# Performance work log

Measured on AMD Instinct MI355X. Metric: run time of the kernel, lower is better.

The kernel has to match this reference:

```python
import jax, jax.numpy as jnp
import numpy as np

IMAGE_SIZE = (128, 128)
NUM_SLICES = 4
SLICE_SPACING = 0.1
BACKGROUND = 0.0
CHUNK = 1024
N_GAUSS = 4096
EPS = 1e-6


def setup_inputs() -> dict:
    key = jax.random.key(0)
    k1, k2, k3, k4, k5 = jax.random.split(key, 5)
    return {
        "means": jax.random.uniform(k1, (N_GAUSS, 3), dtype=jnp.float32),
        "scales": jax.random.uniform(k2, (N_GAUSS, 3), dtype=jnp.float32),
        "rotations": jax.random.normal(k3, (N_GAUSS, 4), dtype=jnp.float32),
        "opacities": jax.random.uniform(k4, (N_GAUSS, 1), dtype=jnp.float32),
        "features": jax.random.uniform(k5, (N_GAUSS, 1), dtype=jnp.float32),
    }


def _quat_to_rot(q):
    # q: [N,4] (w,x,y,z) -> [N,3,3]
    q = q / jnp.linalg.norm(q, axis=1, keepdims=True)
    w, x, y, z = q[:, 0], q[:, 1], q[:, 2], q[:, 3]
    r0 = jnp.stack([1 - 2 * (y * y + z * z), 2 * (x * y - w * z), 2 * (x * z + w * y)], axis=-1)
    r1 = jnp.stack([2 * (x * y + w * z), 1 - 2 * (x * x + z * z), 2 * (y * z - w * x)], axis=-1)
    r2 = jnp.stack([2 * (x * z - w * y), 2 * (y * z + w * x), 1 - 2 * (x * x + y * y)], axis=-1)
    return jnp.stack([r0, r1, r2], axis=-2)


def _forward(means, scales, rotations, opacities, features):
    H, W = IMAGE_SIZE
    dtype = means.dtype
    P = H * W

    # 3D covariance: Sigma = (R S)(R S)^T
    R = _quat_to_rot(rotations)
    RS = R * scales[:, None, :]
    cov = RS @ jnp.swapaxes(RS, 1, 2)  # [N,3,3]

    # slice z positions and shared pixel grid
    total_depth = (NUM_SLICES - 1) * SLICE_SPACING
    zs = jnp.linspace(-total_depth / 2, total_depth / 2, NUM_SLICES)
    yy, xx = jnp.meshgrid(jnp.linspace(-1, 1, H), jnp.linspace(-1, 1, W), indexing="ij")
    grid = jnp.stack([xx, yy], axis=-1).reshape(P, 2).astype(dtype)

    # conditional (marginal-at-z) 2D covariance, slice independent
    sxy = cov[:, :2, :2]                     # [N,2,2]
    sxz = cov[:, :2, 2]                      # [N,2]
    szz = cov[:, 2, 2]                       # [N]
    sigma2d = sxy - (sxz[:, :, None] * sxz[:, None, :]) / (szz + EPS)[:, None, None]
    sigma2d = sigma2d + EPS * jnp.eye(2, dtype=dtype)
    a, b = sigma2d[:, 0, 0], sigma2d[:, 0, 1]
    c, d = sigma2d[:, 1, 0], sigma2d[:, 1, 1]
    det = a * d - b * c
    inv2d = jnp.stack([jnp.stack([d, -b], -1), jnp.stack([-c, a], -1)], -2) / det[:, None, None]

    max_dist = 3.0 * scales[:, 2].max()

    nch = N_GAUSS // CHUNK
    rs = lambda t: t.reshape((nch, CHUNK) + t.shape[1:])
    chunks = (rs(means), rs(inv2d), rs(sxz), rs(szz), rs(opacities[:, 0]), rs(features[:, 0]))

    def render_slice(slice_z):
        def body(carry, ch):
            img, acc = carry
            mu, invk, sxzk, szzk, op, ft = ch
            mask = (jnp.abs(mu[:, 2] - slice_z) < max_dist).astype(dtype)  # all-pass by construction
            zoff = slice_z - mu[:, 2]
            mu2d = mu[:, :2] + sxzk / (szzk + EPS)[:, None] * zoff[:, None]  # [K,2]
            off = grid[:, None, :] - mu2d[None, :, :]                        # [P,K,2]
            maha = jnp.einsum("pki,kij,pkj->pk", off, invk, off)
            g = jnp.exp(-0.5 * maha) * mask[None, :]                         # [P,K]
            weight = (1 - acc)[:, None] * (g * op[None, :])
            img = img + (weight * (g * ft[None, :])).sum(-1)
            acc = acc + weight.sum(-1)
            return (img, acc), None

        init = (jnp.zeros(P, dtype), jnp.zeros(P, dtype))
        (img, acc), _ = jax.lax.scan(body, init, chunks)
        img = img + (1 - acc) * BACKGROUND
        return img.reshape(H, W)

    return jnp.stack([render_slice(zs[s]) for s in range(NUM_SLICES)], axis=0)


def reference(means, scales, rotations, opacities, features):
    return _forward(means, scales, rotations, opacities, features)
```

## Files before the change

### kernel.cpp

```cpp
#include <hip/hip_runtime.h>


#define EPSV 1e-6f
#define NG   4096
#define PP   16384
#define NSL  4
#define SPLIT 8
#define PXW  64
#define GPW  128

__global__ void prep_kernel(const float* __restrict__ means,
                            const float* __restrict__ scales,
                            const float* __restrict__ rots,
                            const float* __restrict__ ops,
                            const float* __restrict__ fts,
                            float4* __restrict__ gdata) {
    __shared__ float red[256];
    int tid = threadIdx.x;

    float m = -1e30f;
    for (int i = tid; i < NG; i += 256) m = fmaxf(m, scales[i*3+2]);
    red[tid] = m;
    __syncthreads();
    for (int s = 128; s > 0; s >>= 1) {
        if (tid < s) red[tid] = fmaxf(red[tid], red[tid+s]);
        __syncthreads();
    }
    float maxd = 3.0f * red[0];

    int g = blockIdx.x * 256 + tid;
    if (g >= NG) return;

    float qw = rots[g*4+0], qx = rots[g*4+1], qy = rots[g*4+2], qz = rots[g*4+3];
    float inorm = rsqrtf(qw*qw + qx*qx + qy*qy + qz*qz);
    qw *= inorm; qx *= inorm; qy *= inorm; qz *= inorm;

    float s0 = scales[g*3+0], s1 = scales[g*3+1], s2 = scales[g*3+2];

    float r00 = 1.f - 2.f*(qy*qy + qz*qz), r01 = 2.f*(qx*qy - qw*qz), r02 = 2.f*(qx*qz + qw*qy);
    float r10 = 2.f*(qx*qy + qw*qz), r11 = 1.f - 2.f*(qx*qx + qz*qz), r12 = 2.f*(qy*qz - qw*qx);
    float r20 = 2.f*(qx*qz - qw*qy), r21 = 2.f*(qy*qz + qw*qx), r22 = 1.f - 2.f*(qx*qx + qy*qy);

    float a00 = r00*s0, a01 = r01*s1, a02 = r02*s2;
    float a10 = r10*s0, a11 = r11*s1, a12 = r12*s2;
    float a20 = r20*s0, a21 = r21*s1, a22 = r22*s2;

    float c00 = a00*a00 + a01*a01 + a02*a02;
    float c01 = a00*a10 + a01*a11 + a02*a12;
    float c02 = a00*a20 + a01*a21 + a02*a22;
    float c11 = a10*a10 + a11*a11 + a12*a12;
    float c12 = a10*a20 + a11*a21 + a12*a22;
    float c22 = a20*a20 + a21*a21 + a22*a22;

    float izz = 1.0f / (c22 + EPSV);
    float kx = c02 * izz, ky = c12 * izz;
    float sa = c00 - c02*c02*izz + EPSV;
    float sb = c01 - c02*c12*izz;
    float sd = c11 - c12*c12*izz + EPSV;
    float det = sa*sd - sb*sb;
    float idet = 1.0f / det;

    const float C0 = -0.72134752044448170f;
    float qa = C0 * sd * idet;
    float qb = C0 * (-2.0f * sb * idet);
    float qd = C0 * sa * idet;

    float mx = means[g*3+0], my = means[g*3+1], mz = means[g*3+2];
    float op = ops[g], ft = fts[g];

    #pragma unroll
    for (int s = 0; s < NSL; ++s) {
        float z = -0.15f + 0.1f * (float)s;
        float zoff = z - mz;
        float m2x = mx + kx * zoff;
        float m2y = my + ky * zoff;
        bool live = (fabsf(mz - z) < maxd) && (op > 1e-12f);
        float lop  = live ? __log2f(op) : -__builtin_inff();
        float ftop = live ? ft / op     : 0.f;
        gdata[(s*NG + g)*2 + 0] = make_float4(m2x, m2y, qa, qb);
        gdata[(s*NG + g)*2 + 1] = make_float4(qd, lop, ftop, 0.f);
    }
}

__global__ __launch_bounds__(512, 8)
void render_kernel(const float4* __restrict__ gdata, float* __restrict__ out) {
    __shared__ float parts[SPLIT][PXW][9];

    int tid   = threadIdx.x;
    int px    = tid & 63;
    int split = __builtin_amdgcn_readfirstlane(tid >> 6);
    int slice = blockIdx.x >> 8;
    int tile  = blockIdx.x & 255;
    int pxg   = tile * PXW + px;
    int row   = pxg >> 7, col = pxg & 127;
    float x = (float)col * (2.0f/127.0f) - 1.0f;
    float y = (float)row * (2.0f/127.0f) - 1.0f;

    const float4* gs = gdata + slice * (NG*2);

    #pragma unroll
    for (int c = 0; c < 4; ++c) {
        const float4* p = gs + (size_t)(c*1024 + split*GPW) * 2;
        float a1 = 0.f, a2 = 0.f;
        #pragma unroll 8
        for (int g = 0; g < GPW; ++g) {
            float4 A = p[2*g+0];
            float4 B = p[2*g+1];
            float dx = x - A.x;
            float dy = y - A.y;
            float t  = fmaf(A.z, dx, A.w * dy);
            float e  = fmaf(B.x * dy, dy, B.y);
            float mm = fmaf(dx, t, e);
            float gv = __builtin_amdgcn_exp2f(mm);
            a1 += gv;
            a2 = fmaf(gv * gv, B.z, a2);
        }
        parts[split][px][c]     = a1;
        parts[split][px][c + 4] = a2;
    }
    __syncthreads();

    if (tid < 64) {
        float img = 0.f, acc = 0.f;
        #pragma unroll
        for (int c = 0; c < 4; ++c) {
            float S1 = 0.f, S2 = 0.f;
            #pragma unroll
            for (int s = 0; s < SPLIT; ++s) {
                S1 += parts[s][px][c];
                S2 += parts[s][px][c + 4];
            }
            float om = 1.0f - acc;
            img = fmaf(om, S2, img);
            acc = fmaf(om, S1, acc);
        }
        out[slice * PP + pxg] = img;
    }
}

extern "C" void kernel_launch(void* const* d_in, const int* in_sizes, int n_in,
                              void* d_out, int out_size, void* d_ws, size_t ws_size,
                              hipStream_t stream) {
    const float* means  = (const float*)d_in[0];
    const float* scales = (const float*)d_in[1];
    const float* rots   = (const float*)d_in[2];
    const float* ops    = (const float*)d_in[3];
    const float* fts    = (const float*)d_in[4];
    float* out = (float*)d_out;

    float4* gdata = (float4*)d_ws;

    prep_kernel<<<NG/256, 256, 0, stream>>>(means, scales, rots, ops, fts, gdata);
    render_kernel<<<NSL*(PP/PXW), 512, 0, stream>>>(gdata, out);
}
```

Measured before the change: 147.7 us.

## Render two pixels per thread with packed float2 math and duplicated Gaussian params

Each thread now handles two pixels in the same row, 64 columns apart, and does the per-Gaussian math on 2-wide float vectors. The aim is to let the compiler emit packed FP32 instructions (v_pk_fma/v_pk_add), halving the ALU instruction count per pixel. The prep kernel stores every parameter duplicated into float2 pairs and negates the means so vector loads feed the packed ops directly. This doubles the Gaussian data footprint (64 bytes per Gaussian per slice) and halves the block count to 512. The launch-bounds occupancy hint is also dropped.

```diff
diff --git a/kernel.cpp b/kernel.cpp
--- a/kernel.cpp
+++ b/kernel.cpp
@@ -6,8 +6,9 @@
 #define PP   16384
 #define NSL  4
 #define SPLIT 8
-#define PXW  64
 #define GPW  128
+
+typedef float v2f __attribute__((ext_vector_type(2)));
 
 __global__ void prep_kernel(const float* __restrict__ means,
                             const float* __restrict__ scales,
@@ -77,64 +78,78 @@
         bool live = (fabsf(mz - z) < maxd) && (op > 1e-12f);
         float lop  = live ? __log2f(op) : -__builtin_inff();
         float ftop = live ? ft / op     : 0.f;
-        gdata[(s*NG + g)*2 + 0] = make_float4(m2x, m2y, qa, qb);
-        gdata[(s*NG + g)*2 + 1] = make_float4(qd, lop, ftop, 0.f);
+        float4* o = gdata + ((size_t)(s*NG + g)) * 4;
+        o[0] = make_float4(-m2x, -m2x, -m2y, -m2y);
+        o[1] = make_float4( qa,   qa,   qb,   qb );
+        o[2] = make_float4( qd,   qd,   lop,  lop);
+        o[3] = make_float4( ftop, ftop, 0.f,  0.f);
     }
 }
 
-__global__ __launch_bounds__(512, 8)
-void render_kernel(const float4* __restrict__ gdata, float* __restrict__ out) {
-    __shared__ float parts[SPLIT][PXW][9];
+__global__ __launch_bounds__(512)
+void render_kernel(const v2f* __restrict__ gdata, float* __restrict__ out) {
+    __shared__ float parts[SPLIT][64][20];
 
     int tid   = threadIdx.x;
-    int px    = tid & 63;
+    int lane  = tid & 63;
     int split = __builtin_amdgcn_readfirstlane(tid >> 6);
-    int slice = blockIdx.x >> 8;
-    int tile  = blockIdx.x & 255;
-    int pxg   = tile * PXW + px;
-    int row   = pxg >> 7, col = pxg & 127;
-    float x = (float)col * (2.0f/127.0f) - 1.0f;
-    float y = (float)row * (2.0f/127.0f) - 1.0f;
+    int slice = blockIdx.x >> 7;
+    int row   = blockIdx.x & 127;
 
-    const float4* gs = gdata + slice * (NG*2);
+    const float DL = 2.0f / 127.0f;
+    float xlo = -1.0f + (float)lane * DL;
+    float y   = -1.0f + (float)row  * DL;
+    v2f xP; xP.x = xlo; xP.y = xlo + 64.0f * DL;
+    v2f yP; yP.x = y;   yP.y = y;
+
+    const v2f* gs = gdata + (size_t)slice * NG * 8;
 
     #pragma unroll
     for (int c = 0; c < 4; ++c) {
-        const float4* p = gs + (size_t)(c*1024 + split*GPW) * 2;
-        float a1 = 0.f, a2 = 0.f;
-        #pragma unroll 8
+        const v2f* p = gs + (size_t)(c * 1024 + split * GPW) * 8;
+        v2f a1 = {0.f, 0.f}, a2 = {0.f, 0.f};
+        #pragma unroll 4
         for (int g = 0; g < GPW; ++g) {
-            float4 A = p[2*g+0];
-            float4 B = p[2*g+1];
-            float dx = x - A.x;
-            float dy = y - A.y;
-            float t  = fmaf(A.z, dx, A.w * dy);
-            float e  = fmaf(B.x * dy, dy, B.y);
-            float mm = fmaf(dx, t, e);
-            float gv = __builtin_amdgcn_exp2f(mm);
+            const v2f* q = p + g * 8;
+            v2f nmx = q[0], nmy = q[1], qa = q[2], qb = q[3];
+            v2f qd  = q[4], lop = q[5], ftp = q[6];
+            v2f dx = xP + nmx;
+            v2f dy = yP + nmy;
+            v2f e  = __builtin_elementwise_fma(qd * dy, dy, lop);
+            v2f t  = __builtin_elementwise_fma(qa, dx, qb * dy);
+            v2f mm = __builtin_elementwise_fma(dx, t, e);
+            v2f gv;
+            gv.x = __builtin_amdgcn_exp2f(mm.x);
+            gv.y = __builtin_amdgcn_exp2f(mm.y);
             a1 += gv;
-            a2 = fmaf(gv * gv, B.z, a2);
+            a2 = __builtin_elementwise_fma(gv * gv, ftp, a2);
         }
-        parts[split][px][c]     = a1;
-        parts[split][px][c + 4] = a2;
+        parts[split][lane][c*4+0] = a1.x;
+        parts[split][lane][c*4+1] = a1.y;
+        parts[split][lane][c*4+2] = a2.x;
+        parts[split][lane][c*4+3] = a2.y;
     }
     __syncthreads();
 
     if (tid < 64) {
-        float img = 0.f, acc = 0.f;
+        float imgl = 0.f, accl = 0.f, imgh = 0.f, acch = 0.f;
         #pragma unroll
         for (int c = 0; c < 4; ++c) {
-            float S1 = 0.f, S2 = 0.f;
+            float S1l = 0.f, S1h = 0.f, S2l = 0.f, S2h = 0.f;
             #pragma unroll
             for (int s = 0; s < SPLIT; ++s) {
-                S1 += parts[s][px][c];
-                S2 += parts[s][px][c + 4];
+                S1l += parts[s][tid][c*4+0];
+                S1h += parts[s][tid][c*4+1];
+                S2l += parts[s][tid][c*4+2];
+                S2h += parts[s][tid][c*4+3];
             }
-            float om = 1.0f - acc;
-            img = fmaf(om, S2, img);
-            acc = fmaf(om, S1, acc);
+            float oml = 1.f - accl, omh = 1.f - acch;
+            imgl = fmaf(oml, S2l, imgl);  accl = fmaf(oml, S1l, accl);
+            imgh = fmaf(omh, S2h, imgh);  acch = fmaf(omh, S1h, acch);
         }
-        out[slice * PP + pxg] = img;
+        int base = slice * PP + row * 128;
+        out[base + tid]      = imgl;
+        out[base + tid + 64] = imgh;
     }
 }
 
@@ -151,5 +166,5 @@
     float4* gdata = (float4*)d_ws;
 
     prep_kernel<<<NG/256, 256, 0, stream>>>(means, scales, rots, ops, fts, gdata);
-    render_kernel<<<NSL*(PP/PXW), 512, 0, stream>>>(gdata, out);
+    render_kernel<<<NSL*128, 512, 0, stream>>>((const v2f*)gdata, out);
 }
```

Result: slower. 157.0 us (+6.3%).

## Register-block four pixels per thread with packed float2 math and 16-way split

Applied to the files above, without the earlier changes.

Each thread now evaluates four pixels (two columns by two rows) per loaded Gaussian using packed two-wide float vector ops. This amortises the shared Gaussian loads and the x/y offset math across pixels. Blocks grow to 1024 threads covering two image rows, with the Gaussian range split 16 ways, and the per-chunk reduction is spread over four waves instead of one. Means are stored negated so the offset becomes an add. The costs are more registers per thread, an extra barrier per chunk, and only 256 blocks in the grid, which may leave the device under-occupied.

```diff
diff --git a/kernel.cpp b/kernel.cpp
--- a/kernel.cpp
+++ b/kernel.cpp
@@ -5,9 +5,12 @@
 #define NG   4096
 #define PP   16384
 #define NSL  4
-#define SPLIT 8
-#define PXW  64
-#define GPW  128
+#define SPLIT 16
+#define GPC  64
+
+typedef float v2f __attribute__((ext_vector_type(2)));
+
+static __device__ __forceinline__ v2f splat(float s) { v2f r; r.x = s; r.y = s; return r; }
 
 __global__ void prep_kernel(const float* __restrict__ means,
                             const float* __restrict__ scales,
@@ -77,65 +80,83 @@
         bool live = (fabsf(mz - z) < maxd) && (op > 1e-12f);
         float lop  = live ? __log2f(op) : -__builtin_inff();
         float ftop = live ? ft / op     : 0.f;
-        gdata[(s*NG + g)*2 + 0] = make_float4(m2x, m2y, qa, qb);
-        gdata[(s*NG + g)*2 + 1] = make_float4(qd, lop, ftop, 0.f);
+        float4* o = gdata + ((size_t)(s*NG + g)) * 2;
+        o[0] = make_float4(-m2x, -m2y, qa, qb);
+        o[1] = make_float4( qd,   lop,  ftop, 0.f);
     }
 }
 
-__global__ __launch_bounds__(512, 8)
+__global__ __launch_bounds__(1024, 4)
 void render_kernel(const float4* __restrict__ gdata, float* __restrict__ out) {
-    __shared__ float parts[SPLIT][PXW][9];
+    __shared__ float parts[SPLIT][64][9];
 
     int tid   = threadIdx.x;
-    int px    = tid & 63;
+    int lane  = tid & 63;
     int split = __builtin_amdgcn_readfirstlane(tid >> 6);
-    int slice = blockIdx.x >> 8;
-    int tile  = blockIdx.x & 255;
-    int pxg   = tile * PXW + px;
-    int row   = pxg >> 7, col = pxg & 127;
-    float x = (float)col * (2.0f/127.0f) - 1.0f;
-    float y = (float)row * (2.0f/127.0f) - 1.0f;
+    int slice = blockIdx.x >> 6;
+    int r0    = (blockIdx.x & 63) * 2;
 
-    const float4* gs = gdata + slice * (NG*2);
+    const float DL = 2.0f / 127.0f;
+    v2f xP;  xP.x = -1.0f + (float)lane * DL;  xP.y = xP.x + 64.0f * DL;
+    v2f yP0 = splat(-1.0f + (float)r0 * DL);
+    v2f yP1 = splat(-1.0f + (float)(r0 + 1) * DL);
+
+    const float4* gs = gdata + (size_t)slice * NG * 2;
+
+    float img = 0.f, acc = 0.f;
 
     #pragma unroll
     for (int c = 0; c < 4; ++c) {
-        const float4* p = gs + (size_t)(c*1024 + split*GPW) * 2;
-        float a1 = 0.f, a2 = 0.f;
+        const float4* p = gs + (size_t)(c * 1024 + split * GPC) * 2;
+        v2f a10 = {0.f,0.f}, a11 = {0.f,0.f}, a20 = {0.f,0.f}, a21 = {0.f,0.f};
         #pragma unroll 8
-        for (int g = 0; g < GPW; ++g) {
+        for (int g = 0; g < GPC; ++g) {
             float4 A = p[2*g+0];
             float4 B = p[2*g+1];
-            float dx = x - A.x;
-            float dy = y - A.y;
-            float t  = fmaf(A.z, dx, A.w * dy);
-            float e  = fmaf(B.x * dy, dy, B.y);
-            float mm = fmaf(dx, t, e);
-            float gv = __builtin_amdgcn_exp2f(mm);
-            a1 += gv;
-            a2 = fmaf(gv * gv, B.z, a2);
+            v2f dx  = xP  + splat(A.x);
+            v2f dy0 = yP0 + splat(A.y);
+            v2f dy1 = yP1 + splat(A.y);
+            v2f t0  = __builtin_elementwise_fma(splat(A.z), dx, splat(A.w) * dy0);
+            v2f t1  = __builtin_elementwise_fma(splat(A.z), dx, splat(A.w) * dy1);
+            v2f e0  = __builtin_elementwise_fma(splat(B.x) * dy0, dy0, splat(B.y));
+            v2f e1  = __builtin_elementwise_fma(splat(B.x) * dy1, dy1, splat(B.y));
+            v2f mm0 = __builtin_elementwise_fma(dx, t0, e0);
+            v2f mm1 = __builtin_elementwise_fma(dx, t1, e1);
+            v2f gv0, gv1;
+            gv0.x = __builtin_amdgcn_exp2f(mm0.x);
+            gv0.y = __builtin_amdgcn_exp2f(mm0.y);
+            gv1.x = __builtin_amdgcn_exp2f(mm1.x);
+            gv1.y = __builtin_amdgcn_exp2f(mm1.y);
+            a10 += gv0;
+            a11 += gv1;
+            a20 = __builtin_elementwise_fma(gv0 * gv0, splat(B.z), a20);
+            a21 = __builtin_elementwise_fma(gv1 * gv1, splat(B.z), a21);
         }
-        parts[split][px][c]     = a1;
-        parts[split][px][c + 4] = a2;
-    }
-    __syncthreads();
-
-    if (tid < 64) {
-        float img = 0.f, acc = 0.f;
-        #pragma unroll
-        for (int c = 0; c < 4; ++c) {
+        __syncthreads();
+        parts[split][lane][0] = a10.x;
+        parts[split][lane][1] = a10.y;
+        parts[split][lane][2] = a11.x;
+        parts[split][lane][3] = a11.y;
+        parts[split][lane][4] = a20.x;
+        parts[split][lane][5] = a20.y;
+        parts[split][lane][6] = a21.x;
+        parts[split][lane][7] = a21.y;
+        __syncthreads();
+        if (split < 4) {
             float S1 = 0.f, S2 = 0.f;
             #pragma unroll
             for (int s = 0; s < SPLIT; ++s) {
-                S1 += parts[s][px][c];
-                S2 += parts[s][px][c + 4];
+                S1 += parts[s][lane][split];
+                S2 += parts[s][lane][4 + split];
             }
             float om = 1.0f - acc;
             img = fmaf(om, S2, img);
             acc = fmaf(om, S1, acc);
         }
-        out[slice * PP + pxg] = img;
     }
+
+    if (split < 4)
+        out[slice * PP + (r0 + (split >> 1)) * 128 + (split & 1) * 64 + lane] = img;
 }
 
 extern "C" void kernel_launch(void* const* d_in, const int* in_sizes, int n_in,
@@ -151,5 +172,5 @@
     float4* gdata = (float4*)d_ws;
 
     prep_kernel<<<NG/256, 256, 0, stream>>>(means, scales, rots, ops, fts, gdata);
-    render_kernel<<<NSL*(PP/PXW), 512, 0, stream>>>(gdata, out);
+    render_kernel<<<NSL*64, 1024, 0, stream>>>(gdata, out);
 }
```

Result: faster. 130.7 us (-11.5%).
